# Kernel tuning notes

Hardware: AMD Instinct MI355X
Metric: run time of the kernel (lower is better)

The kernel has to match this reference:

```python
import jax, jax.numpy as jnp
import numpy as np

# Forest of B perfect binary trees, depth D levels, M = 2**D - 1 nodes/tree.
B, D, H, X, VOCAB, NCLS = 32, 12, 256, 256, 32000, 20
M = 2 ** D - 1          # 4095 nodes per tree
N = B * M               # 131040 total nodes


def setup_inputs() -> dict:
    key = jax.random.key(0)
    ks = jax.random.split(key, 9)
    x = jax.random.randint(ks[0], (N,), 0, VOCAB, dtype=jnp.int32)
    # leaves are the last level of each tree: in-tree index >= 2**(D-1)-1
    leaf = (jnp.arange(M) >= 2 ** (D - 1) - 1).astype(jnp.int32)
    x_mask = jnp.tile(leaf, B)  # [N] int32, 1 on leaves, 0 on internal nodes
    s = 0.02
    Emb = jax.random.normal(ks[1], (VOCAB, X), jnp.float32) * s
    W_iou = jax.random.normal(ks[2], (3 * H, X), jnp.float32) * s
    b_iou = jnp.zeros((3 * H,), jnp.float32)
    U_iou = jax.random.normal(ks[3], (3 * H, H), jnp.float32) * s
    U_f = jax.random.normal(ks[4], (H, H), jnp.float32) * s
    b_f = jnp.ones((H,), jnp.float32)  # forget-gate bias init
    W_out = jax.random.normal(ks[5], (NCLS, H), jnp.float32) * s
    b_out = jnp.zeros((NCLS,), jnp.float32)
    return {"x": x, "x_mask": x_mask, "Emb": Emb, "W_iou": W_iou,
            "b_iou": b_iou, "U_iou": U_iou, "U_f": U_f, "b_f": b_f,
            "W_out": W_out, "b_out": b_out}


def reference(x, x_mask, Emb, W_iou, b_iou, U_iou, U_f, b_f, W_out, b_out):
    # input_module: embedding applied to masked ids, result masked again
    x_emb = Emb[x * x_mask] * x_mask[:, None].astype(Emb.dtype)      # [N, X]
    xiou = (x_emb @ W_iou.T).reshape(B, M, 3 * H)                    # W_iou * x per node
    h_sum = jnp.zeros((B, M, H), Emb.dtype)    # sum of children h (childsum)
    fc_sum = jnp.zeros((B, M, H), Emb.dtype)   # sum_k f_k * c_k from children
    h_all = jnp.zeros((B, M, H), Emb.dtype)
    # topological propagation: leaves (deepest level) -> roots
    for l in range(D - 1, -1, -1):
        s_, e_ = 2 ** l - 1, 2 ** (l + 1) - 1  # static in-tree level slice
        iou = xiou[:, s_:e_] + h_sum[:, s_:e_] @ U_iou.T + b_iou
        i, o, u = jnp.split(iou, 3, axis=-1)
        c = jax.nn.sigmoid(i) * jnp.tanh(u) + fc_sum[:, s_:e_]
        h = jax.nn.sigmoid(o) * jnp.tanh(c)
        h_all = h_all.at[:, s_:e_].set(h)
        if l > 0:
            f = jax.nn.sigmoid(h @ U_f.T + b_f)          # per-child forget gate
            parents = (np.arange(s_, e_) - 1) // 2       # static parent indices
            h_sum = h_sum.at[:, parents].add(h)
            fc_sum = fc_sum.at[:, parents].add(f * c)
    # output_module applied to all node states
    return h_all.reshape(N, H) @ W_out.T + b_out                    # [N, NCLS]
```

## Files before the change

kernel.cpp:

```cpp
#include <hip/hip_runtime.h>

#define B_TREES 32
#define DEPTH   12
#define M_NODES 4095
#define N_NODES (B_TREES * M_NODES)
#define HDIM    256
#define VOCAB   32000
#define NCLS    20
#define LEAFROWS 65536
#define LDSH_S 20

typedef _Float16 f16;
typedef _Float16 f16x8 __attribute__((ext_vector_type(8)));
typedef _Float16 f16x4 __attribute__((ext_vector_type(4)));
typedef _Float16 f16x2 __attribute__((ext_vector_type(2)));
typedef float    f32x4 __attribute__((ext_vector_type(4)));

__device__ __forceinline__ float sigf(float x)      { return 1.0f / (1.0f + __expf(-x)); }
__device__ __forceinline__ float tanh_fast(float x) { return 1.0f - 2.0f / (1.0f + __expf(2.0f * x)); }

__global__ __launch_bounds__(256) void cvt_kernel(
    const float4* __restrict__ Emb,  const float4* __restrict__ Wiou,
    const float4* __restrict__ Uiou, const float4* __restrict__ Uf,
    const float4* __restrict__ Wout,
    f16x4* __restrict__ Emb16,  f16x4* __restrict__ Wiou16,
    f16x4* __restrict__ Uiou16, f16x4* __restrict__ Uf16,
    f16x4* __restrict__ Wout16)
{
    int i = blockIdx.x * 256 + threadIdx.x;
    if (i < VOCAB * HDIM / 4) {
        float4 v = Emb[i];
        f16x4 r; r[0] = (f16)v.x; r[1] = (f16)v.y; r[2] = (f16)v.z; r[3] = (f16)v.w;
        Emb16[i] = r;
    }
    if (i < 768 * HDIM / 4) {
        float4 v = Wiou[i];
        f16x4 r; r[0] = (f16)v.x; r[1] = (f16)v.y; r[2] = (f16)v.z; r[3] = (f16)v.w;
        Wiou16[i] = r;
        float4 u = Uiou[i];
        f16x4 s; s[0] = (f16)u.x; s[1] = (f16)u.y; s[2] = (f16)u.z; s[3] = (f16)u.w;
        Uiou16[i] = s;
    }
    if (i < HDIM * HDIM / 4) {
        float4 v = Uf[i];
        f16x4 r; r[0] = (f16)v.x; r[1] = (f16)v.y; r[2] = (f16)v.z; r[3] = (f16)v.w;
        Uf16[i] = r;
    }
    if (i < 32 * HDIM / 4) {
        int row = i >> 6;
        f16x4 r = {};
        if (row < NCLS) {
            float4 v = Wout[i];
            r[0] = (f16)v.x; r[1] = (f16)v.y; r[2] = (f16)v.z; r[3] = (f16)v.w;
        }
        Wout16[i] = r;
    }
}

#define LEAF_TPW 16
__global__ __launch_bounds__(256) void leaf_kernel(
    const int* __restrict__ x, const f16* __restrict__ Emb16,
    const f16* __restrict__ Wiou16, const float* __restrict__ b_iou,
    f16* __restrict__ h16, f16* __restrict__ cT)
{
    __shared__ f16 wlds[1536 * 8];
    __shared__ f16 ldsh[4][16 * LDSH_S];

    const int tid  = threadIdx.x;
    const int lane = tid & 63;
    const int w    = tid >> 6;
    const int quad = lane >> 4;
    const int l15  = lane & 15;
    const int qk   = quad * 8;
    const int cb0  = blockIdx.y * 16;

    #pragma unroll
    for (int i = 0; i < 6; ++i) {
        int f = i * 256 + tid;
        int mat = f >> 9, r = f & 511, ks = r >> 6, q = (r >> 4) & 3, c = r & 15;
        *(f16x8*)(wlds + f * 8) = *(const f16x8*)(Wiou16 +
            (mat * 256 + cb0 + c) * HDIM + ks * 32 + q * 8);
    }
    __syncthreads();

    const float bi = b_iou[cb0 + l15];
    const float bo = b_iou[256 + cb0 + l15];
    const float bu = b_iou[512 + cb0 + l15];

    const int row0 = (blockIdx.x * 4 + w) * (LEAF_TPW * 16);

    int nodeRow = (row0 >> 11) * M_NODES + 2047 + (row0 & 2047);
    int embBase = x[nodeRow + l15] * HDIM;
    f16x8 a[8];
    #pragma unroll
    for (int ks = 0; ks < 8; ++ks)
        a[ks] = *(const f16x8*)(Emb16 + embBase + ks * 32 + qk);

    for (int rt = 0; rt < LEAF_TPW; ++rt) {
        const int rw = row0 + rt * 16;
        const int curNode = nodeRow;
        f16x8 ac[8];
        #pragma unroll
        for (int ks = 0; ks < 8; ++ks) ac[ks] = a[ks];

        if (rt + 1 < LEAF_TPW) {
            const int rwn = rw + 16;
            nodeRow = (rwn >> 11) * M_NODES + 2047 + (rwn & 2047);
            embBase = x[nodeRow + l15] * HDIM;
            #pragma unroll
            for (int ks = 0; ks < 8; ++ks)
                a[ks] = *(const f16x8*)(Emb16 + embBase + ks * 32 + qk);
        }

        f32x4 acc[3] = {};
        #pragma unroll
        for (int ks = 0; ks < 8; ++ks) {
            #pragma unroll
            for (int mat = 0; mat < 3; ++mat) {
                f16x8 wf = *(const f16x8*)(wlds +
                    ((mat * 8 + ks) * 64 + quad * 16 + l15) * 8);
                acc[mat] = __builtin_amdgcn_mfma_f32_16x16x32_f16(
                    ac[ks], wf, acc[mat], 0, 0, 0);
            }
        }

        f16x4 cv;
        #pragma unroll
        for (int r = 0; r < 4; ++r) {
            float i_ = acc[0][r] + bi;
            float o_ = acc[1][r] + bo;
            float u_ = acc[2][r] + bu;
            float c  = sigf(i_) * tanh_fast(u_);
            float h  = sigf(o_) * tanh_fast(c);
            cv[r] = (f16)c;
            ldsh[w][(quad * 4 + r) * LDSH_S + l15] = (f16)h;
        }
        *(f16x4*)(cT + (cb0 + l15) * LEAFROWS + rw + quad * 4) = cv;

        {
            int row_l = lane >> 2, cpos = (lane & 3) * 4;
            f16x4 v = *(const f16x4*)(&ldsh[w][row_l * LDSH_S + cpos]);
            *(f16x4*)(h16 + (curNode + row_l) * HDIM + cb0 + cpos) = v;
        }
    }
}

template <bool STAGE>
__global__ __launch_bounds__(256) void fused_level_kernel(
    const f16* __restrict__ Uiou16, const f16* __restrict__ Uf16,
    const float* __restrict__ b_iou, const float* __restrict__ b_f,
    f16* __restrict__ h16, const f16* __restrict__ cT_child,
    f16* __restrict__ cT_parent, int l, int rows_p, int tpw)
{
    __shared__ f16 wlds[STAGE ? 2048 * 8 : 8];
    __shared__ f16 ldsh[4][16 * LDSH_S];

    const int tid  = threadIdx.x;
    const int lane = tid & 63;
    const int w    = tid >> 6;
    const int quad = lane >> 4;
    const int l15  = lane & 15;
    const int qk   = quad * 8;
    const int cb0  = blockIdx.y * 16;

    if (STAGE) {
        #pragma unroll
        for (int i = 0; i < 8; ++i) {
            int f = i * 256 + tid;
            int mat = f >> 9, r = f & 511, ks = r >> 6, q = (r >> 4) & 3, c = r & 15;
            const f16* src = (mat == 0)
                ? (Uf16 + (cb0 + c) * HDIM + ks * 32 + q * 8)
                : (Uiou16 + ((mat - 1) * 256 + cb0 + c) * HDIM + ks * 32 + q * 8);
            *(f16x8*)(wlds + f * 8) = *(const f16x8*)src;
        }
        __syncthreads();
    }

    const float bi  = b_iou[cb0 + l15];
    const float bo  = b_iou[256 + cb0 + l15];
    const float bu  = b_iou[512 + cb0 + l15];
    const float bfv = b_f[cb0 + l15];
    const int lc = l + 1;
    const int maskc = (1 << lc) - 1;
    const int maskp = (1 << l) - 1;
    const int rows_c = rows_p * 2;

    const int p0 = blockIdx.x * (tpw * 64);

    for (int pt = 0; pt < tpw; ++pt) {
        const int pw = p0 + (pt * 4 + w) * 16;
        if (pw >= rows_p) continue;
        const int cw = 2 * pw;

        int childBase0, childBase1;
        {
            int cl0 = cw + l15;
            childBase0 = ((cl0 >> lc) * M_NODES + maskc + (cl0 & maskc)) * HDIM;
            int cl1 = cw + 16 + l15;
            childBase1 = ((cl1 >> lc) * M_NODES + maskc + (cl1 & maskc)) * HDIM;
        }

        f32x4 accf0 = {}, accf1 = {};
        f32x4 au0[3] = {}, au1[3] = {};
        #pragma unroll
        for (int ks = 0; ks < 8; ++ks) {
            const int k0 = ks * 32 + qk;
            f16x8 a0 = *(const f16x8*)(h16 + childBase0 + k0);
            f16x8 a1 = *(const f16x8*)(h16 + childBase1 + k0);
            f16x8 wfF = STAGE
                ? *(const f16x8*)(wlds + (ks * 64 + quad * 16 + l15) * 8)
                : *(const f16x8*)(Uf16 + (cb0 + l15) * HDIM + k0);
            accf0 = __builtin_amdgcn_mfma_f32_16x16x32_f16(a0, wfF, accf0, 0, 0, 0);
            accf1 = __builtin_amdgcn_mfma_f32_16x16x32_f16(a1, wfF, accf1, 0, 0, 0);
            #pragma unroll
            for (int m = 0; m < 3; ++m) {
                f16x8 wm = STAGE
                    ? *(const f16x8*)(wlds + (((m + 1) * 8 + ks) * 64 + quad * 16 + l15) * 8)
                    : *(const f16x8*)(Uiou16 + (m * 256 + cb0 + l15) * HDIM + k0);
                au0[m] = __builtin_amdgcn_mfma_f32_16x16x32_f16(a0, wm, au0[m], 0, 0, 0);
                au1[m] = __builtin_amdgcn_mfma_f32_16x16x32_f16(a1, wm, au1[m], 0, 0, 0);
            }
        }

        #pragma unroll
        for (int s = 0; s < 2; ++s) {
            const f32x4& af = s ? accf1 : accf0;
            const f32x4* au = s ? au1 : au0;
            const int csr = cw + s * 16;
            f16x4 cc = *(const f16x4*)(cT_child +
                (cb0 + l15) * rows_c + csr + quad * 4);
            f16x2 cpack;
            #pragma unroll
            for (int pr = 0; pr < 2; ++pr) {
                float f0 = sigf(af[2 * pr]     + bfv);
                float f1 = sigf(af[2 * pr + 1] + bfv);
                float fc = f0 * (float)cc[2 * pr] + f1 * (float)cc[2 * pr + 1];
                float i_ = au[0][2 * pr] + au[0][2 * pr + 1] + bi;
                float o_ = au[1][2 * pr] + au[1][2 * pr + 1] + bo;
                float u_ = au[2][2 * pr] + au[2][2 * pr + 1] + bu;
                float c  = sigf(i_) * tanh_fast(u_) + fc;
                float h  = sigf(o_) * tanh_fast(c);
                cpack[pr] = (f16)c;
                ldsh[w][(s * 8 + quad * 2 + pr) * LDSH_S + l15] = (f16)h;
            }
            *(f16x2*)(cT_parent + (cb0 + l15) * rows_p + pw + s * 8 + quad * 2) = cpack;
        }

        {
            int prow = lane >> 2, cpos = (lane & 3) * 4;
            int p = pw + prow;
            int b = p >> l, tt = p & maskp;
            int node = b * M_NODES + (1 << l) - 1 + tt;
            f16x4 v = *(const f16x4*)(&ldsh[w][prow * LDSH_S + cpos]);
            *(f16x4*)(h16 + node * HDIM + cb0 + cpos) = v;
        }
    }
}

__global__ __launch_bounds__(256) void out_kernel(
    const f16* __restrict__ h16, const f16* __restrict__ Wout16,
    const float* __restrict__ bout, float* __restrict__ out)
{
    const int lane = threadIdx.x & 63;
    const int w    = threadIdx.x >> 6;
    const int quad = lane >> 4;
    const int l15  = lane & 15;
    const int qk   = quad * 8;

    f16x8 wfk[2][8];
    #pragma unroll
    for (int cf = 0; cf < 2; ++cf)
        #pragma unroll
        for (int ks = 0; ks < 8; ++ks)
            wfk[cf][ks] = *(const f16x8*)(Wout16 +
                (cf * 16 + l15) * HDIM + ks * 32 + qk);
    float bo[2];
    #pragma unroll
    for (int cf = 0; cf < 2; ++cf) {
        int col = cf * 16 + l15;
        bo[cf] = bout[col < NCLS ? col : 0];
    }

    const int ntotal = N_NODES / 16;
    const int t0     = blockIdx.x * 16 + w * 4;
    const int tn     = (t0 >= ntotal) ? 0 : ((ntotal - t0 < 4) ? ntotal - t0 : 4);
    if (tn <= 0) return;

    f16x8 a[8];
    #pragma unroll
    for (int ks = 0; ks < 8; ++ks)
        a[ks] = *(const f16x8*)(h16 + (t0 * 16 + l15) * HDIM + ks * 32 + qk);

    for (int i = 0; i < tn; ++i) {
        const int rw = (t0 + i) * 16;
        f16x8 ac[8];
        #pragma unroll
        for (int ks = 0; ks < 8; ++ks) ac[ks] = a[ks];

        {
            const int tnx = (i + 1 < tn) ? t0 + i + 1 : t0 + i;
            #pragma unroll
            for (int ks = 0; ks < 8; ++ks)
                a[ks] = *(const f16x8*)(h16 + (tnx * 16 + l15) * HDIM + ks * 32 + qk);
        }

        f32x4 acc[2] = {};
        #pragma unroll
        for (int ks = 0; ks < 8; ++ks)
            #pragma unroll
            for (int cf = 0; cf < 2; ++cf)
                acc[cf] = __builtin_amdgcn_mfma_f32_16x16x32_f16(
                    ac[ks], wfk[cf][ks], acc[cf], 0, 0, 0);

        #pragma unroll
        for (int cf = 0; cf < 2; ++cf) {
            const int col = cf * 16 + l15;
            if (col < NCLS) {
                #pragma unroll
                for (int r = 0; r < 4; ++r)
                    out[(rw + quad * 4 + r) * NCLS + col] = acc[cf][r] + bo[cf];
            }
        }
    }
}

extern "C" void kernel_launch(void* const* d_in, const int* in_sizes, int n_in,
                              void* d_out, int out_size, void* d_ws, size_t ws_size,
                              hipStream_t stream)
{
    const int*   x     = (const int*)d_in[0];
    const float* Emb   = (const float*)d_in[2];
    const float* W_iou = (const float*)d_in[3];
    const float* b_iou = (const float*)d_in[4];
    const float* U_iou = (const float*)d_in[5];
    const float* U_f   = (const float*)d_in[6];
    const float* b_f   = (const float*)d_in[7];
    const float* W_out = (const float*)d_in[8];
    const float* b_out = (const float*)d_in[9];
    float* out = (float*)d_out;

    char* ws = (char*)d_ws;
    size_t off = 0;
    auto take = [&](size_t bytes) -> char* {
        char* p = ws + off; off += (bytes + 255) & ~(size_t)255; return p;
    };
    f16* h16    = (f16*)take((size_t)N_NODES * HDIM * 2);
    f16* cA     = (f16*)take((size_t)HDIM * LEAFROWS * 2);
    f16* cB     = (f16*)take((size_t)HDIM * (LEAFROWS / 2) * 2);
    f16* Emb16  = (f16*)take((size_t)VOCAB * HDIM * 2);
    f16* Wiou16 = (f16*)take((size_t)768 * HDIM * 2);
    f16* Uiou16 = (f16*)take((size_t)768 * HDIM * 2);
    f16* Uf16   = (f16*)take((size_t)HDIM * HDIM * 2);
    f16* Wout16 = (f16*)take((size_t)32 * HDIM * 2);

    cvt_kernel<<<VOCAB * HDIM / 4 / 256, 256, 0, stream>>>(
        (const float4*)Emb, (const float4*)W_iou, (const float4*)U_iou,
        (const float4*)U_f, (const float4*)W_out,
        (f16x4*)Emb16, (f16x4*)Wiou16, (f16x4*)Uiou16, (f16x4*)Uf16,
        (f16x4*)Wout16);

    leaf_kernel<<<dim3(LEAFROWS / (4 * 16 * LEAF_TPW), 16), 256, 0, stream>>>(
        x, Emb16, Wiou16, b_iou, h16, cA);

    f16* cin  = cA;
    f16* cout_ = cB;
    for (int l = 10; l >= 0; --l) {
        int rows_p = B_TREES << l;
        int tpw    = rows_p / 4096; if (tpw < 1) tpw = 1;
        int gx     = (rows_p + tpw * 64 - 1) / (tpw * 64);
        if (rows_p >= 8192)
            fused_level_kernel<true><<<dim3(gx, 16), 256, 0, stream>>>(
                Uiou16, Uf16, b_iou, b_f, h16, cin, cout_, l, rows_p, tpw);
        else
            fused_level_kernel<false><<<dim3(gx, 16), 256, 0, stream>>>(
                Uiou16, Uf16, b_iou, b_f, h16, cin, cout_, l, rows_p, tpw);
        f16* t = cin; cin = cout_; cout_ = t;
    }

    out_kernel<<<dim3((N_NODES / 16 + 15) / 16), 256, 0, stream>>>(
        h16, Wout16, b_out, out);
}
```

Before: 420.8 us.

## Widen per-warp tile to 32 parents and always stage weights in LDS

Each warp in the per-level kernel now handles 32 parent rows (64 children, four 16-row MFMA tiles) instead of 16. Each weight fragment read from LDS therefore feeds four MFMAs instead of two. Weight staging into LDS now runs at every level rather than only the large ones, and the grid and rows-per-block arithmetic change to match. In exchange the kernel holds more accumulator registers, launches fewer blocks on small levels, and drops the padding on the h staging buffer, which may cause LDS bank conflicts.

```diff
diff --git a/kernel.cpp b/kernel.cpp
--- a/kernel.cpp
+++ b/kernel.cpp
@@ -145,15 +145,14 @@
     }
 }
 
-template <bool STAGE>
 __global__ __launch_bounds__(256) void fused_level_kernel(
     const f16* __restrict__ Uiou16, const f16* __restrict__ Uf16,
     const float* __restrict__ b_iou, const float* __restrict__ b_f,
     f16* __restrict__ h16, const f16* __restrict__ cT_child,
     f16* __restrict__ cT_parent, int l, int rows_p, int tpw)
 {
-    __shared__ f16 wlds[STAGE ? 2048 * 8 : 8];
-    __shared__ f16 ldsh[4][16 * LDSH_S];
+    __shared__ f16 wlds[2048 * 8];
+    __shared__ f16 ldsh[4][32 * 16];
 
     const int tid  = threadIdx.x;
     const int lane = tid & 63;
@@ -163,18 +162,16 @@
     const int qk   = quad * 8;
     const int cb0  = blockIdx.y * 16;
 
-    if (STAGE) {
-        #pragma unroll
-        for (int i = 0; i < 8; ++i) {
-            int f = i * 256 + tid;
-            int mat = f >> 9, r = f & 511, ks = r >> 6, q = (r >> 4) & 3, c = r & 15;
-            const f16* src = (mat == 0)
-                ? (Uf16 + (cb0 + c) * HDIM + ks * 32 + q * 8)
-                : (Uiou16 + ((mat - 1) * 256 + cb0 + c) * HDIM + ks * 32 + q * 8);
-            *(f16x8*)(wlds + f * 8) = *(const f16x8*)src;
-        }
-        __syncthreads();
-    }
+    #pragma unroll
+    for (int i = 0; i < 8; ++i) {
+        int f = i * 256 + tid;
+        int mat = f >> 9, r = f & 511, ks = r >> 6, q = (r >> 4) & 3, c = r & 15;
+        const f16* src = (mat == 0)
+            ? (Uf16 + (cb0 + c) * HDIM + ks * 32 + q * 8)
+            : (Uiou16 + ((mat - 1) * 256 + cb0 + c) * HDIM + ks * 32 + q * 8);
+        *(f16x8*)(wlds + f * 8) = *(const f16x8*)src;
+    }
+    __syncthreads();
 
     const float bi  = b_iou[cb0 + l15];
     const float bo  = b_iou[256 + cb0 + l15];
@@ -185,74 +182,76 @@
     const int maskp = (1 << l) - 1;
     const int rows_c = rows_p * 2;
 
-    const int p0 = blockIdx.x * (tpw * 64);
+    const int p0 = blockIdx.x * (tpw * 128);
 
     for (int pt = 0; pt < tpw; ++pt) {
-        const int pw = p0 + (pt * 4 + w) * 16;
+        const int pw = p0 + (pt * 4 + w) * 32;
         if (pw >= rows_p) continue;
         const int cw = 2 * pw;
 
-        int childBase0, childBase1;
-        {
-            int cl0 = cw + l15;
-            childBase0 = ((cl0 >> lc) * M_NODES + maskc + (cl0 & maskc)) * HDIM;
-            int cl1 = cw + 16 + l15;
-            childBase1 = ((cl1 >> lc) * M_NODES + maskc + (cl1 & maskc)) * HDIM;
-        }
-
-        f32x4 accf0 = {}, accf1 = {};
-        f32x4 au0[3] = {}, au1[3] = {};
+        int childBase[4];
+        #pragma unroll
+        for (int s = 0; s < 4; ++s) {
+            int cl = cw + s * 16 + l15;
+            childBase[s] = ((cl >> lc) * M_NODES + maskc + (cl & maskc)) * HDIM;
+        }
+        f16x4 cc[4];
+        #pragma unroll
+        for (int s = 0; s < 4; ++s)
+            cc[s] = *(const f16x4*)(cT_child +
+                (cb0 + l15) * rows_c + cw + s * 16 + quad * 4);
+
+        f32x4 accf[4] = {};
+        f32x4 au[3][4] = {};
         #pragma unroll
         for (int ks = 0; ks < 8; ++ks) {
             const int k0 = ks * 32 + qk;
-            f16x8 a0 = *(const f16x8*)(h16 + childBase0 + k0);
-            f16x8 a1 = *(const f16x8*)(h16 + childBase1 + k0);
-            f16x8 wfF = STAGE
-                ? *(const f16x8*)(wlds + (ks * 64 + quad * 16 + l15) * 8)
-                : *(const f16x8*)(Uf16 + (cb0 + l15) * HDIM + k0);
-            accf0 = __builtin_amdgcn_mfma_f32_16x16x32_f16(a0, wfF, accf0, 0, 0, 0);
-            accf1 = __builtin_amdgcn_mfma_f32_16x16x32_f16(a1, wfF, accf1, 0, 0, 0);
+            f16x8 a[4];
+            #pragma unroll
+            for (int s = 0; s < 4; ++s)
+                a[s] = *(const f16x8*)(h16 + childBase[s] + k0);
+            f16x8 wfF = *(const f16x8*)(wlds + (ks * 64 + quad * 16 + l15) * 8);
+            #pragma unroll
+            for (int s = 0; s < 4; ++s)
+                accf[s] = __builtin_amdgcn_mfma_f32_16x16x32_f16(
+                    a[s], wfF, accf[s], 0, 0, 0);
             #pragma unroll
             for (int m = 0; m < 3; ++m) {
-                f16x8 wm = STAGE
-                    ? *(const f16x8*)(wlds + (((m + 1) * 8 + ks) * 64 + quad * 16 + l15) * 8)
-                    : *(const f16x8*)(Uiou16 + (m * 256 + cb0 + l15) * HDIM + k0);
-                au0[m] = __builtin_amdgcn_mfma_f32_16x16x32_f16(a0, wm, au0[m], 0, 0, 0);
-                au1[m] = __builtin_amdgcn_mfma_f32_16x16x32_f16(a1, wm, au1[m], 0, 0, 0);
+                f16x8 wm = *(const f16x8*)(wlds +
+                    (((m + 1) * 8 + ks) * 64 + quad * 16 + l15) * 8);
+                #pragma unroll
+                for (int s = 0; s < 4; ++s)
+                    au[m][s] = __builtin_amdgcn_mfma_f32_16x16x32_f16(
+                        a[s], wm, au[m][s], 0, 0, 0);
             }
         }
 
         #pragma unroll
-        for (int s = 0; s < 2; ++s) {
-            const f32x4& af = s ? accf1 : accf0;
-            const f32x4* au = s ? au1 : au0;
-            const int csr = cw + s * 16;
-            f16x4 cc = *(const f16x4*)(cT_child +
-                (cb0 + l15) * rows_c + csr + quad * 4);
+        for (int s = 0; s < 4; ++s) {
             f16x2 cpack;
             #pragma unroll
             for (int pr = 0; pr < 2; ++pr) {
-                float f0 = sigf(af[2 * pr]     + bfv);
-                float f1 = sigf(af[2 * pr + 1] + bfv);
-                float fc = f0 * (float)cc[2 * pr] + f1 * (float)cc[2 * pr + 1];
-                float i_ = au[0][2 * pr] + au[0][2 * pr + 1] + bi;
-                float o_ = au[1][2 * pr] + au[1][2 * pr + 1] + bo;
-                float u_ = au[2][2 * pr] + au[2][2 * pr + 1] + bu;
+                float f0 = sigf(accf[s][2 * pr]     + bfv);
+                float f1 = sigf(accf[s][2 * pr + 1] + bfv);
+                float fc = f0 * (float)cc[s][2 * pr] + f1 * (float)cc[s][2 * pr + 1];
+                float i_ = au[0][s][2 * pr] + au[0][s][2 * pr + 1] + bi;
+                float o_ = au[1][s][2 * pr] + au[1][s][2 * pr + 1] + bo;
+                float u_ = au[2][s][2 * pr] + au[2][s][2 * pr + 1] + bu;
                 float c  = sigf(i_) * tanh_fast(u_) + fc;
                 float h  = sigf(o_) * tanh_fast(c);
                 cpack[pr] = (f16)c;
-                ldsh[w][(s * 8 + quad * 2 + pr) * LDSH_S + l15] = (f16)h;
+                ldsh[w][(s * 8 + quad * 2 + pr) * 16 + l15] = (f16)h;
             }
             *(f16x2*)(cT_parent + (cb0 + l15) * rows_p + pw + s * 8 + quad * 2) = cpack;
         }
 
         {
-            int prow = lane >> 2, cpos = (lane & 3) * 4;
+            int prow = lane >> 1, cpos = (lane & 1) * 8;
             int p = pw + prow;
             int b = p >> l, tt = p & maskp;
             int node = b * M_NODES + (1 << l) - 1 + tt;
-            f16x4 v = *(const f16x4*)(&ldsh[w][prow * LDSH_S + cpos]);
-            *(f16x4*)(h16 + node * HDIM + cb0 + cpos) = v;
+            f16x8 v = *(const f16x8*)(&ldsh[w][prow * 16 + cpos]);
+            *(f16x8*)(h16 + node * HDIM + cb0 + cpos) = v;
         }
     }
 }
@@ -366,14 +365,10 @@
     f16* cout_ = cB;
     for (int l = 10; l >= 0; --l) {
         int rows_p = B_TREES << l;
-        int tpw    = rows_p / 4096; if (tpw < 1) tpw = 1;
-        int gx     = (rows_p + tpw * 64 - 1) / (tpw * 64);
-        if (rows_p >= 8192)
-            fused_level_kernel<true><<<dim3(gx, 16), 256, 0, stream>>>(
-                Uiou16, Uf16, b_iou, b_f, h16, cin, cout_, l, rows_p, tpw);
-        else
-            fused_level_kernel<false><<<dim3(gx, 16), 256, 0, stream>>>(
-                Uiou16, Uf16, b_iou, b_f, h16, cin, cout_, l, rows_p, tpw);
+        int tpw    = rows_p / 16384; if (tpw < 1) tpw = 1;
+        int gx     = (rows_p + tpw * 128 - 1) / (tpw * 128);
+        fused_level_kernel<<<dim3(gx, 16), 256, 0, stream>>>(
+            Uiou16, Uf16, b_iou, b_f, h16, cin, cout_, l, rows_p, tpw);
         f16* t = cin; cin = cout_; cout_ = t;
     }
 
```

After: 422.0 us. Within noise of the previous version (+0.3%).
